# Optimization experiments

Hardware: AMD Instinct MI355X
Metric: run time of the kernel (lower is better)

The kernel has to match this reference:

```python
import jax, jax.numpy as jnp
import numpy as np

# ---- geometry / physics constants (from setup_params) ----
H = 400; W_CROP = 400
PSF_W = 121          # interpolated_psf_width
CLEAR = 20           # clear_dist
_m = int(np.ceil(PSF_W / 2 - CLEAR + 2))
MARGIN = _m + _m % 2                    # 44
IM = H + 2 * MARGIN                     # 488
MAG = 100.0; PX_CCD = 11.0              # M, pixel_size_CCD
NZ = 64; Z_MIN = -2.0; Z_MAX = 2.0      # psf bank z sampling
SIGMA_READ = 10.0                       # read noise std (counts)
N_EMIT = 2048


def setup_inputs() -> dict:
    key = jax.random.key(0)
    k1, k2, k3, k4 = jax.random.split(key, 4)
    # emitter positions (um): xy in [-15,15] (stays inside canvas), z in [-2,2]
    lo = jnp.array([-15.0, -15.0, Z_MIN], jnp.float32)
    hi = jnp.array([15.0, 15.0, Z_MAX], jnp.float32)
    local_xyz = jax.random.uniform(k1, (1, N_EMIT, 3), jnp.float32) * (hi - lo) + lo
    Nphotons = jax.random.uniform(k2, (1, N_EMIT), jnp.float32) * 4000.0 + 1000.0
    xy_center = jnp.zeros((2,), jnp.float32)  # FOV center; unused when fd_flag=False
    psf_bank = jax.random.uniform(k3, (NZ, PSF_W, PSF_W), jnp.float32)  # positive PSFs
    noise_map = jax.random.normal(k4, (H, W_CROP), jnp.float32)         # unit gaussians
    return {"local_xyz": local_xyz, "Nphotons": Nphotons, "xy_center": xy_center,
            "psf_bank": psf_bank, "noise_map": noise_map}


def reference(local_xyz, Nphotons, xy_center, psf_bank, noise_map):
    x = local_xyz[0, :, 0]                       # [N] um
    y = local_xyz[0, :, 1]
    z = local_xyz[0, :, 2]
    nph = Nphotons[0]                            # [N]

    # psf_module(0,0,z): nearest-z lookup in precomputed bank (fd_flag=False)
    zi = jnp.clip(jnp.round((z - Z_MIN) / (Z_MAX - Z_MIN) * (NZ - 1)),
                  0, NZ - 1).astype(jnp.int32)
    psf = psf_bank[zi]                           # [N, PSF_W, PSF_W]

    # emitter position in camera pixels
    lx = x * MAG / PX_CCD
    ly = y * MAG / PX_CCD
    r0f = ly + IM / 2 - PSF_W / 2
    c0f = lx + IM / 2 - PSF_W / 2
    r0 = jnp.floor(r0f).astype(jnp.int32)        # [N] integer splat origin
    c0 = jnp.floor(c0f).astype(jnp.int32)
    rs = (r0f - jnp.floor(r0f))[:, None, None]   # sub-pixel shift in [0,1)
    cs = (c0f - jnp.floor(c0f))[:, None, None]

    # sub-pixel shift (bilinear, zero-fill boundary): out[i,j] = in[i-rs, j-cs]
    P = jnp.pad(psf, ((0, 0), (1, 0), (1, 0)))
    sh = ((1 - rs) * (1 - cs) * P[:, 1:, 1:] + rs * (1 - cs) * P[:, :-1, 1:]
          + (1 - rs) * cs * P[:, 1:, :-1] + rs * cs * P[:, :-1, :-1])
    sh = jnp.abs(sh)
    sh = sh / sh.sum(axis=(1, 2), keepdims=True) * nph[:, None, None]

    # scatter-add splat into shared canvas
    ar = jnp.arange(PSF_W, dtype=jnp.int32)
    rows = r0[:, None, None] + ar[None, :, None]  # [N, PSF_W, 1]
    cols = c0[:, None, None] + ar[None, None, :]  # [N, 1, PSF_W]
    canvas = jnp.zeros((IM, IM), sh.dtype).at[rows, cols].add(sh)

    im = canvas[MARGIN:MARGIN + H, MARGIN:MARGIN + W_CROP]

    # NoiseLayer: Gaussian approx of Poisson shot + read noise
    im_noisy = im + jnp.sqrt(jnp.maximum(im, 0.0) + SIGMA_READ ** 2) * noise_map

    # project_01 normalization
    return (im_noisy - im_noisy.min()) / (im_noisy.max() - im_noisy.min())
```

## Files before the change

### kernel.cpp

```cpp
#include <hip/hip_runtime.h>

#define H        400
#define W_CROP   400
#define PSF_W    121
#define MARGIN   44
#define IM       488
#define NZ       64
#define N_EMIT   2048
#define PSF_AREA (PSF_W * PSF_W)
#define SIGMA2   100.0f
#define TILE     16
#define TB       25
#define NTILES   (TB * TB)
#define NPIX     (H * W_CROP)
#define PADW     152
#define PADA     (PADW * PADW)
#define CHUNKS   4
#define CAPC     224
#define CAP_B    512
#define NBUCK    (TB * CHUNKS)
#define PADBLK   512

typedef __fp16 h2 __attribute__((ext_vector_type(2)));

#if __has_builtin(__builtin_amdgcn_fdot2)
#define FDOT2(a, b, c) __builtin_amdgcn_fdot2((a), (b), (c), false)
#else
static __device__ __forceinline__ float FDOT2(h2 a, h2 b, float c) {
    return fmaf((float)a.x, (float)b.x, fmaf((float)a.y, (float)b.y, c));
}
#endif

static __device__ __forceinline__ unsigned pkh2(float lo, float hi) {
    const h2 v = __builtin_amdgcn_cvt_pkrtz(lo, hi);
    return __builtin_bit_cast(unsigned, v);
}

static __device__ __forceinline__ unsigned enc_ord(float f) {
    unsigned u = __float_as_uint(f);
    return (u & 0x80000000u) ? ~u : (u | 0x80000000u);
}
static __device__ __forceinline__ float dec_ord(unsigned u) {
    return __uint_as_float((u & 0x80000000u) ? (u & 0x7fffffffu) : ~u);
}

static __device__ __forceinline__ void geom_of(const float* __restrict__ xyz, int e,
                                               int& r0, int& c0, int& zi,
                                               float& r0f, float& c0f) {
    const float x = xyz[3 * e + 0];
    const float y = xyz[3 * e + 1];
    const float z = xyz[3 * e + 2];
    const float lx = (x * 100.0f) / 11.0f;
    const float ly = (y * 100.0f) / 11.0f;
    r0f = (ly + 244.0f) - 60.5f;
    c0f = (lx + 244.0f) - 60.5f;
    r0 = (int)floorf(r0f);
    c0 = (int)floorf(c0f);
    zi = (int)rintf((z + 2.0f) / 4.0f * 63.0f);
    zi = min(max(zi, 0), NZ - 1);
}

__global__ __launch_bounds__(256) void prep_kernel(
        const float* __restrict__ psf_bank, float* __restrict__ zpart,
        unsigned* __restrict__ pad, unsigned* __restrict__ minmax,
        const float* __restrict__ xyz, const float* __restrict__ nph_arr,
        float4* __restrict__ bucket, int* __restrict__ bcnt)
{
    __shared__ float red[4][4];
    __shared__ int   wtot[4];

    if (blockIdx.x < PADBLK) {
        const int zi   = blockIdx.x >> 3;
        const int part = blockIdx.x & 7;

        if (blockIdx.x == 0 && threadIdx.x == 0) { minmax[0] = 0xFFFFFFFFu; minmax[1] = 0u; }

        const float* __restrict__ src = psf_bank + (size_t)zi * PSF_AREA;
        unsigned* __restrict__ dst = pad + (size_t)zi * PADA;

        const int plo = part * 2888;
        const int phi = min(plo + 2888, PADA);
        for (int i = plo + (int)threadIdx.x; i < phi; i += 256) {
            const int rp = i / PADW;
            const int r = rp - 16;
            const int c = i - rp * PADW - 16;
            const bool rin = (unsigned)r < (unsigned)PSF_W;
            const float vm = (rin && (unsigned)(c - 1) < 120u)           ? src[r * PSF_W + c - 1] : 0.0f;
            const float vc = (rin && (unsigned)c < (unsigned)PSF_W)      ? src[r * PSF_W + c]     : 0.0f;
            dst[i] = pkh2(vm, vc);
        }

        const int slo = part * 1831;
        const int shi = min(slo + 1831, PSF_AREA);
        float S = 0.f, R = 0.f, C = 0.f, K = 0.f;
        for (int i = slo + (int)threadIdx.x; i < shi; i += 256) {
            const float v = src[i];
            const int r = i / PSF_W;
            const int c = i - r * PSF_W;
            S += v;
            if (r == PSF_W - 1) R += v;
            if (c == PSF_W - 1) C += v;
            if (r == PSF_W - 1 && c == PSF_W - 1) K += v;
        }
        #pragma unroll
        for (int off = 32; off > 0; off >>= 1) {
            S += __shfl_down(S, off, 64);
            R += __shfl_down(R, off, 64);
            C += __shfl_down(C, off, 64);
            K += __shfl_down(K, off, 64);
        }
        const int wave = threadIdx.x >> 6, lane = threadIdx.x & 63;
        if (lane == 0) { red[wave][0] = S; red[wave][1] = R; red[wave][2] = C; red[wave][3] = K; }
        __syncthreads();
        if (threadIdx.x == 0) {
            float4 o;
            o.x = (red[0][0] + red[1][0]) + (red[2][0] + red[3][0]);
            o.y = (red[0][1] + red[1][1]) + (red[2][1] + red[3][1]);
            o.z = (red[0][2] + red[1][2]) + (red[2][2] + red[3][2]);
            o.w = (red[0][3] + red[1][3]) + (red[2][3] + red[3][3]);
            *(float4*)(zpart + (size_t)(zi * 8 + part) * 4) = o;
        }
        return;
    }

    const int b   = blockIdx.x - PADBLK;
    const int btr = b >> 2, bzc = b & 3;
    const int w    = threadIdx.x >> 6;
    const int lane = threadIdx.x & 63;

    int mycnt = 0;
    unsigned mymask = 0u;
    #pragma unroll
    for (int q = 0; q < 8; ++q) {
        const int e = (int)threadIdx.x * 8 + q;
        int r0, c0, zi; float r0f, c0f;
        geom_of(xyz, e, r0, c0, zi, r0f, c0f);
        const bool p = ((zi >> 4) == bzc)
                     && (btr >= ((r0 - MARGIN) >> 4)) && (btr <= ((r0 + 76) >> 4));
        mymask |= (unsigned)p << q;
        mycnt += (int)p;
    }

    int incl = mycnt;
    #pragma unroll
    for (int off = 1; off < 64; off <<= 1) {
        const int v = __shfl_up(incl, off, 64);
        if (lane >= off) incl += v;
    }
    if (lane == 63) wtot[w] = incl;
    __syncthreads();
    int base = incl - mycnt;
    #pragma unroll
    for (int ww = 0; ww < 4; ++ww) base += (ww < w) ? wtot[ww] : 0;
    const int ntot = wtot[0] + wtot[1] + wtot[2] + wtot[3];

    if (mymask) {
        int slot = base;
        #pragma unroll
        for (int q = 0; q < 8; ++q) {
            if (mymask & (1u << q)) {
                const int e = (int)threadIdx.x * 8 + q;
                int r0, c0, zi; float r0f, c0f;
                geom_of(xyz, e, r0, c0, zi, r0f, c0f);
                if (slot < CAP_B) {
                    const float rs = r0f - floorf(r0f);
                    const float cs = c0f - floorf(c0f);
                    const float nph = nph_arr[e];
                    float4 s0, s1;
                    s0.x = nph * (1.0f - rs) * (1.0f - cs);
                    s0.y = nph * (1.0f - rs) * cs;
                    s0.z = nph * rs * (1.0f - cs);
                    s0.w = nph * rs * cs;
                    const int packed = ((r0 + 16) << 15) | ((c0 + 16) << 6) | zi;
                    s1.x = rs; s1.y = cs; s1.z = __int_as_float(packed); s1.w = 0.f;
                    bucket[(size_t)(b * CAP_B + slot) * 2]     = s0;
                    bucket[(size_t)(b * CAP_B + slot) * 2 + 1] = s1;
                }
                ++slot;
            }
        }
    }
    if (threadIdx.x == 0) bcnt[b] = min(ntot, CAP_B);
}

__global__ __launch_bounds__(256) void gather_kernel(
        const unsigned* __restrict__ pad, const float4* __restrict__ bucket,
        const int* __restrict__ bcnt, const float* __restrict__ zpart,
        float* __restrict__ parts)
{
    const int zc   = (blockIdx.x & 7) >> 1;
    const int tile = 2 * (blockIdx.x >> 3) + (blockIdx.x & 1);
    if (tile >= NTILES) return;

    __shared__ float4 smeta[CAPC];
    __shared__ float  tilepart[4][256];
    __shared__ int    wtot[4];

    const int tr = tile / TB, tc = tile - tr * TB;
    const int w    = threadIdx.x >> 6;
    const int lane = threadIdx.x & 63;
    const int px = lane & 15;
    const int wy = lane >> 4;
    const int orow0 = tr * TILE + wy * 4;
    const int ocol  = tc * TILE + px;
    const int crow0 = orow0 + MARGIN;
    const int ccol  = ocol + MARGIN;
    const int tcb   = (crow0 * PADW + ccol) * 4;
    const char* __restrict__ pbase = (const char*)pad;

    const int b   = tr * CHUNKS + zc;
    const int n_b = bcnt[b];
    const float4* __restrict__ bk = bucket + (size_t)b * CAP_B * 2;

    int nstaged = 0;
    for (int base_i = 0; base_i < n_b; base_i += 256) {
        const int i = base_i + (int)threadIdx.x;
        float4 m0, m1;
        int r0 = 0, c0 = 0, zi = 0;
        bool p = false;
        if (i < n_b) {
            m0 = bk[2 * i];
            m1 = bk[2 * i + 1];
            const int packed = __float_as_int(m1.z);
            zi = packed & 63;
            c0 = ((packed >> 6) & 511) - 16;
            r0 = ((packed >> 15) & 511) - 16;
            p = (tc >= ((c0 - MARGIN) >> 4)) && (tc <= ((c0 + 76) >> 4));
        }
        int incl = (int)p;
        #pragma unroll
        for (int off = 1; off < 64; off <<= 1) {
            const int v = __shfl_up(incl, off, 64);
            if (lane >= off) incl += v;
        }
        if (lane == 63) wtot[w] = incl;
        __syncthreads();
        int slot = nstaged + incl - (int)p;
        #pragma unroll
        for (int ww = 0; ww < 4; ++ww) slot += (ww < w) ? wtot[ww] : 0;
        const int round_tot = wtot[0] + wtot[1] + wtot[2] + wtot[3];
        if (p && slot < CAPC) {
            const float rs = m1.x, cs = m1.y;
            const float4* __restrict__ zp = (const float4*)zpart + zi * 8;
            float4 zm = zp[0];
            #pragma unroll
            for (int u = 1; u < 8; ++u) {
                const float4 t = zp[u];
                zm.x += t.x; zm.y += t.y; zm.z += t.z; zm.w += t.w;
            }
            const float ssum = zm.x - rs * zm.y - cs * zm.z + rs * cs * zm.w;
            const float inv = 1.0f / ssum;
            float4 s;
            s.x = __uint_as_float(pkh2(m0.y * inv, m0.x * inv));
            s.y = __uint_as_float(pkh2(m0.w * inv, m0.z * inv));
            s.z = __int_as_float((zi * PADA + (15 - r0) * PADW + (16 - c0)) * 4);
            s.w = __int_as_float(((r0 + 16) << 16) | (c0 + 16));
            smeta[slot] = s;
        }
        nstaged += round_tot;
        __syncthreads();
    }
    const int n = min(nstaged, CAPC);

    float acc0[4] = {0.f, 0.f, 0.f, 0.f};
    float acc1[4] = {0.f, 0.f, 0.f, 0.f};
    float acc2[4] = {0.f, 0.f, 0.f, 0.f};
    float acc3[4] = {0.f, 0.f, 0.f, 0.f};

    auto body = [&](int j, float* acc) {
        const float4 s = smeta[j];
        const h2 wA = __builtin_bit_cast(h2, s.x);
        const h2 wB = __builtin_bit_cast(h2, s.y);
        const int off = __float_as_int(s.z);
        const int rc  = __float_as_int(s.w);
        const int pr0 = crow0 - ((rc >> 16) - 16);
        const char* __restrict__ p = pbase + (tcb + off);
        h2 f[5];
        #pragma unroll
        for (int i = 0; i < 5; ++i)
            f[i] = __builtin_bit_cast(h2, *(const unsigned*)(p + i * (PADW * 4)));
        #pragma unroll
        for (int k = 0; k < 4; ++k) {
            float v = FDOT2(wA, f[k + 1], 0.0f);
            v = FDOT2(wB, f[k], v);
            acc[k] += (pr0 + k != 121) ? v : 0.f;
        }
    };

    int j = w;
    for (; j + 12 < n; j += 16) {
        body(j, acc0); body(j + 4, acc1); body(j + 8, acc2); body(j + 12, acc3);
    }
    for (; j < n; j += 4) body(j, acc0);

    #pragma unroll
    for (int k = 0; k < 4; ++k)
        tilepart[w][(wy * 4 + k) * 16 + px] = (acc0[k] + acc1[k]) + (acc2[k] + acc3[k]);
    __syncthreads();

    const int row = threadIdx.x >> 4, col = threadIdx.x & 15;
    const float s = ((tilepart[0][threadIdx.x] + tilepart[1][threadIdx.x]) +
                     (tilepart[2][threadIdx.x] + tilepart[3][threadIdx.x]));
    parts[(size_t)zc * NPIX + (tr * TILE + row) * W_CROP + (tc * TILE + col)] = s;
}

__global__ __launch_bounds__(256) void noise_minmax_kernel(
        const float* __restrict__ parts, const float* __restrict__ noise,
        float* __restrict__ out, unsigned* __restrict__ minmax)
{
    const int i = blockIdx.x * 256 + threadIdx.x;
    float vmin = 1e30f, vmax = -1e30f;
    if (i < NPIX / 4) {
        const float4 p0 = ((const float4*)parts)[i];
        const float4 p1 = ((const float4*)(parts + NPIX))[i];
        const float4 p2 = ((const float4*)(parts + 2 * NPIX))[i];
        const float4 p3 = ((const float4*)(parts + 3 * NPIX))[i];
        float4 im;
        im.x = (p0.x + p1.x) + (p2.x + p3.x);
        im.y = (p0.y + p1.y) + (p2.y + p3.y);
        im.z = (p0.z + p1.z) + (p2.z + p3.z);
        im.w = (p0.w + p1.w) + (p2.w + p3.w);
        const float4 nz = ((const float4*)noise)[i];
        im.x += sqrtf(fmaxf(im.x, 0.f) + SIGMA2) * nz.x;
        im.y += sqrtf(fmaxf(im.y, 0.f) + SIGMA2) * nz.y;
        im.z += sqrtf(fmaxf(im.z, 0.f) + SIGMA2) * nz.z;
        im.w += sqrtf(fmaxf(im.w, 0.f) + SIGMA2) * nz.w;
        ((float4*)out)[i] = im;
        vmin = fminf(fminf(im.x, im.y), fminf(im.z, im.w));
        vmax = fmaxf(fmaxf(im.x, im.y), fmaxf(im.z, im.w));
    }
    #pragma unroll
    for (int off = 32; off > 0; off >>= 1) {
        vmin = fminf(vmin, __shfl_down(vmin, off, 64));
        vmax = fmaxf(vmax, __shfl_down(vmax, off, 64));
    }
    if ((threadIdx.x & 63) == 0) {
        atomicMin(&minmax[0], enc_ord(vmin));
        atomicMax(&minmax[1], enc_ord(vmax));
    }
}

__global__ __launch_bounds__(256) void finalize_kernel(float* __restrict__ out,
                                                       const unsigned* __restrict__ minmax)
{
    const int i = blockIdx.x * 256 + threadIdx.x;
    if (i >= NPIX / 4) return;
    const float mn = dec_ord(minmax[0]);
    const float inv = 1.0f / (dec_ord(minmax[1]) - mn);
    float4 v = ((float4*)out)[i];
    v.x = (v.x - mn) * inv;
    v.y = (v.y - mn) * inv;
    v.z = (v.z - mn) * inv;
    v.w = (v.w - mn) * inv;
    ((float4*)out)[i] = v;
}

extern "C" void kernel_launch(void* const* d_in, const int* in_sizes, int n_in,
                              void* d_out, int out_size, void* d_ws, size_t ws_size,
                              hipStream_t stream) {
    const float* xyz      = (const float*)d_in[0];
    const float* nph      = (const float*)d_in[1];
    const float* psf_bank = (const float*)d_in[3];
    const float* noise    = (const float*)d_in[4];
    float* out = (float*)d_out;

    char* ws = (char*)d_ws;
    unsigned* minmax = (unsigned*)(ws + 0);
    float*    zpart  = (float*)(ws + 1024);
    unsigned* pad    = (unsigned*)(ws + 9216);
    float4*   bucket = (float4*)(ws + 5923840);
    int*      bcnt   = (int*)(ws + 7562240);
    float*    parts  = (float*)(ws + 7563264);

    prep_kernel<<<PADBLK + NBUCK, 256, 0, stream>>>(psf_bank, zpart, pad, minmax,
                                                    xyz, nph, bucket, bcnt);
    gather_kernel<<<2504, 256, 0, stream>>>(pad, bucket, bcnt, zpart, parts);
    noise_minmax_kernel<<<(NPIX / 4 + 255) / 256, 256, 0, stream>>>(parts, noise, out, minmax);
    finalize_kernel<<<(NPIX / 4 + 255) / 256, 256, 0, stream>>>(out, minmax);
}
```

Measured before the change: 55.14 us.

## Split PSF pad prep into more blocks and pre-reduce z sums in shared memory

Doubles the number of prep blocks per z-plane (16 parts instead of 8), so each block pads and sums a smaller slice and the grid spreads the prep work more widely. In the gather kernel, the per-z partial sums for the block's z-chunk are reduced once into shared memory with a 16-lane shuffle, instead of each staged emitter reading and adding its own global partials. The wave prefix scan used for compaction is replaced by a ballot plus popcount. Workspace offsets are shifted to fit the larger zpart array, and the extra shared-memory reduction adds a barrier at the start of every gather block.

New measurement: 54.66 us. Within noise of the previous version (-0.9%).

```diff
diff --git a/kernel.cpp b/kernel.cpp
--- a/kernel.cpp
+++ b/kernel.cpp
@@ -19,7 +19,8 @@
 #define CAPC     224
 #define CAP_B    512
 #define NBUCK    (TB * CHUNKS)
-#define PADBLK   512
+#define PADBLK   1024
+#define PPART    16
 
 typedef __fp16 h2 __attribute__((ext_vector_type(2)));
 
@@ -70,16 +71,16 @@
     __shared__ int   wtot[4];
 
     if (blockIdx.x < PADBLK) {
-        const int zi   = blockIdx.x >> 3;
-        const int part = blockIdx.x & 7;
+        const int zi   = blockIdx.x >> 4;
+        const int part = blockIdx.x & 15;
 
         if (blockIdx.x == 0 && threadIdx.x == 0) { minmax[0] = 0xFFFFFFFFu; minmax[1] = 0u; }
 
         const float* __restrict__ src = psf_bank + (size_t)zi * PSF_AREA;
         unsigned* __restrict__ dst = pad + (size_t)zi * PADA;
 
-        const int plo = part * 2888;
-        const int phi = min(plo + 2888, PADA);
+        const int plo = part * 1444;
+        const int phi = min(plo + 1444, PADA);
         for (int i = plo + (int)threadIdx.x; i < phi; i += 256) {
             const int rp = i / PADW;
             const int r = rp - 16;
@@ -90,8 +91,8 @@
             dst[i] = pkh2(vm, vc);
         }
 
-        const int slo = part * 1831;
-        const int shi = min(slo + 1831, PSF_AREA);
+        const int slo = part * 916;
+        const int shi = min(slo + 916, PSF_AREA);
         float S = 0.f, R = 0.f, C = 0.f, K = 0.f;
         for (int i = slo + (int)threadIdx.x; i < shi; i += 256) {
             const float v = src[i];
@@ -118,7 +119,7 @@
             o.y = (red[0][1] + red[1][1]) + (red[2][1] + red[3][1]);
             o.z = (red[0][2] + red[1][2]) + (red[2][2] + red[3][2]);
             o.w = (red[0][3] + red[1][3]) + (red[2][3] + red[3][3]);
-            *(float4*)(zpart + (size_t)(zi * 8 + part) * 4) = o;
+            *(float4*)(zpart + (size_t)(zi * PPART + part) * 4) = o;
         }
         return;
     }
@@ -193,6 +194,7 @@
     if (tile >= NTILES) return;
 
     __shared__ float4 smeta[CAPC];
+    __shared__ float4 szm[16];
     __shared__ float  tilepart[4][256];
     __shared__ int    wtot[4];
 
@@ -207,6 +209,21 @@
     const int ccol  = ocol + MARGIN;
     const int tcb   = (crow0 * PADW + ccol) * 4;
     const char* __restrict__ pbase = (const char*)pad;
+
+    {
+        const int zl = threadIdx.x >> 4;
+        const int pt = threadIdx.x & 15;
+        float4 v = ((const float4*)zpart)[(zc * 16 + zl) * PPART + pt];
+        #pragma unroll
+        for (int off = 8; off > 0; off >>= 1) {
+            v.x += __shfl_down(v.x, off, 16);
+            v.y += __shfl_down(v.y, off, 16);
+            v.z += __shfl_down(v.z, off, 16);
+            v.w += __shfl_down(v.w, off, 16);
+        }
+        if (pt == 0) szm[zl] = v;
+    }
+    __syncthreads();
 
     const int b   = tr * CHUNKS + zc;
     const int n_b = bcnt[b];
@@ -227,27 +244,17 @@
             r0 = ((packed >> 15) & 511) - 16;
             p = (tc >= ((c0 - MARGIN) >> 4)) && (tc <= ((c0 + 76) >> 4));
         }
-        int incl = (int)p;
-        #pragma unroll
-        for (int off = 1; off < 64; off <<= 1) {
-            const int v = __shfl_up(incl, off, 64);
-            if (lane >= off) incl += v;
-        }
-        if (lane == 63) wtot[w] = incl;
+        const unsigned long long m = __ballot(p);
+        const int before = __popcll(m & ((1ULL << lane) - 1ULL));
+        if (lane == 63) wtot[w] = before + (int)p;
         __syncthreads();
-        int slot = nstaged + incl - (int)p;
+        int slot = nstaged + before;
         #pragma unroll
         for (int ww = 0; ww < 4; ++ww) slot += (ww < w) ? wtot[ww] : 0;
         const int round_tot = wtot[0] + wtot[1] + wtot[2] + wtot[3];
         if (p && slot < CAPC) {
             const float rs = m1.x, cs = m1.y;
-            const float4* __restrict__ zp = (const float4*)zpart + zi * 8;
-            float4 zm = zp[0];
-            #pragma unroll
-            for (int u = 1; u < 8; ++u) {
-                const float4 t = zp[u];
-                zm.x += t.x; zm.y += t.y; zm.z += t.z; zm.w += t.w;
-            }
+            const float4 zm = szm[zi & 15];
             const float ssum = zm.x - rs * zm.y - cs * zm.z + rs * cs * zm.w;
             const float inv = 1.0f / ssum;
             float4 s;
@@ -367,10 +374,10 @@
     char* ws = (char*)d_ws;
     unsigned* minmax = (unsigned*)(ws + 0);
     float*    zpart  = (float*)(ws + 1024);
-    unsigned* pad    = (unsigned*)(ws + 9216);
-    float4*   bucket = (float4*)(ws + 5923840);
-    int*      bcnt   = (int*)(ws + 7562240);
-    float*    parts  = (float*)(ws + 7563264);
+    unsigned* pad    = (unsigned*)(ws + 17408);
+    float4*   bucket = (float4*)(ws + 5932032);
+    int*      bcnt   = (int*)(ws + 7570432);
+    float*    parts  = (float*)(ws + 7571456);
 
     prep_kernel<<<PADBLK + NBUCK, 256, 0, stream>>>(psf_bank, zpart, pad, minmax,
                                                     xyz, nph, bucket, bcnt);
```
